# Performance work log

Measured on AMD Instinct MI355X. Metric: run time of the kernel, lower is better.

The kernel has to match this reference:

```python
import jax, jax.numpy as jnp
import numpy as np

EPS = 1e-8  # cosine-similarity epsilon (torch default)


def setup_inputs() -> dict:
    key = jax.random.key(0)
    k1, k2, k3 = jax.random.split(key, 3)
    B, T, D = 256, 512, 512
    video_embedding = jax.random.normal(k1, (B, T, D), dtype=jnp.float32)
    sentence_embedding = jax.random.normal(k2, (B, D), dtype=jnp.float32)
    # valid lengths in [16, T] so no row is fully masked (softmax stays finite)
    video_lengths = jax.random.randint(k3, (B,), 16, T + 1, dtype=jnp.int32)
    return {
        "video_embedding": video_embedding,
        "sentence_embedding": sentence_embedding,
        "video_lengths": video_lengths,
    }


def reference(video_embedding, sentence_embedding, video_lengths):
    B, T, D = video_embedding.shape
    # cosine similarity between every video frame and every sentence -> [B, B, T]
    vn = video_embedding / jnp.maximum(
        jnp.linalg.norm(video_embedding, axis=-1, keepdims=True), EPS)
    sn = sentence_embedding / jnp.maximum(
        jnp.linalg.norm(sentence_embedding, axis=-1, keepdims=True), EPS)
    sim = jnp.einsum("btd,jd->bjt", vn, sn)  # [B_video, B_sent, T]
    # length mask: frames t >= video_lengths[i] get -inf (vectorized version of
    # the original nested python loop)
    valid = jnp.arange(T)[None, None, :] < video_lengths[:, None, None]  # [B,1,T]
    masked = jnp.where(valid, sim, -jnp.inf)
    similarity = jax.nn.softmax(masked, axis=2)  # [B, B, T]
    # argmax over frames, take the diagonal (matched video/sentence pair)
    max_arg = jnp.argmax(similarity, axis=2)       # [B, B]
    diag = jnp.diagonal(max_arg)                   # [B]
    video_max = jnp.take_along_axis(
        video_embedding, diag[:, None, None], axis=1)[:, 0, :]  # [B, D]
    return similarity, video_max
```

## Files before the change

### kernel.cpp

```cpp
#include <hip/hip_runtime.h>
#include <hip/hip_bf16.h>
#include <cstdint>

constexpr int NB = 256;
constexpr int NT = 512;
constexpr int ND = 512;

typedef __attribute__((ext_vector_type(8))) short bf16x8;
typedef __attribute__((ext_vector_type(4))) float f32x4;
typedef __attribute__((ext_vector_type(4))) unsigned int u32x4;

__device__ __forceinline__ float wred_sum(float v){
#pragma unroll
  for (int m = 32; m > 0; m >>= 1) v += __shfl_xor(v, m, 64);
  return v;
}
__device__ __forceinline__ unsigned int f2bf(float f){
  unsigned int u = __builtin_bit_cast(unsigned int, f);
  u = u + 0x7fffu + ((u >> 16) & 1u);
  return (u >> 16);
}
__device__ __forceinline__ void gload_lds16(const void* g, void* l){
  __builtin_amdgcn_global_load_lds(
      (const __attribute__((address_space(1))) unsigned int*)g,
      (__attribute__((address_space(3))) unsigned int*)l, 16, 0, 0);
}

__global__ __launch_bounds__(256) void k_sent(const float* __restrict__ s,
                                              unsigned short* __restrict__ sb,
                                              float* __restrict__ sinv){
  int row  = blockIdx.x * 4 + (threadIdx.x >> 6);
  int lane = threadIdx.x & 63;
  const float* sr = s + (size_t)row * ND;
  float x[8]; float ss = 0.f;
#pragma unroll
  for (int e = 0; e < 8; e++){ x[e] = sr[lane + e*64]; ss += x[e]*x[e]; }
  ss = wred_sum(ss);
  float inv = 1.0f / fmaxf(sqrtf(ss), 1e-8f);
#pragma unroll
  for (int e = 0; e < 8; e++)
    sb[(size_t)row*ND + lane + e*64] = (unsigned short)f2bf(x[e]*inv);
  if (lane == 0) sinv[row] = inv;
}

__global__ __launch_bounds__(256) void k_vnorm(const float* __restrict__ video,
                                               const float* __restrict__ sent,
                                               const float* __restrict__ sinv,
                                               unsigned short* __restrict__ vb16,
                                               float* __restrict__ diag){
  const int tid  = threadIdx.x;
  const int row  = blockIdx.x * 4 + (tid >> 6);
  const int lane = tid & 63;
  const int b    = row >> 9;
  __shared__ float sRowS[ND];
  sRowS[tid]       = sent[(size_t)b*ND + tid];
  sRowS[tid + 256] = sent[(size_t)b*ND + 256 + tid];
  __syncthreads();

  const float* vr = video + (size_t)row * ND;
  f32x4 x0 = *reinterpret_cast<const f32x4*>(vr + lane*8);
  f32x4 x1 = *reinterpret_cast<const f32x4*>(vr + lane*8 + 4);
  float ss = 0.f, dp = 0.f;
#pragma unroll
  for (int i = 0; i < 4; i++){
    ss += x0[i]*x0[i] + x1[i]*x1[i];
    dp += x0[i]*sRowS[lane*8 + i] + x1[i]*sRowS[lane*8 + 4 + i];
  }
#pragma unroll
  for (int m = 32; m > 0; m >>= 1){
    ss += __shfl_xor(ss, m, 64);
    dp += __shfl_xor(dp, m, 64);
  }
  float inv = 1.0f / fmaxf(sqrtf(ss), 1e-8f);
  if (lane == 0) diag[row] = dp * inv * sinv[b];
  u32x4 d;
  d[0] = f2bf(x0[0]*inv) | (f2bf(x0[1]*inv) << 16);
  d[1] = f2bf(x0[2]*inv) | (f2bf(x0[3]*inv) << 16);
  d[2] = f2bf(x1[0]*inv) | (f2bf(x1[1]*inv) << 16);
  d[3] = f2bf(x1[2]*inv) | (f2bf(x1[3]*inv) << 16);
  *reinterpret_cast<u32x4*>(vb16 + (size_t)row*ND + lane*8) = d;
}

__global__ __launch_bounds__(512, 4) void k_gemm_sm(
    const unsigned short* __restrict__ sb,
    const unsigned short* __restrict__ vb16,
    const int* __restrict__ lens,
    float* __restrict__ out0){
  const int tid  = threadIdx.x;
  const int lane = tid & 63;
  const int w    = tid >> 6;
  const int wj   = w >> 2;
  const int wt   = w & 3;

  const int D  = blockIdx.x;
  const int x8 = D & 7;
  const int r0 = D >> 3;
  const int s  = r0 & 3;
  const int b  = (r0 >> 2) * 8 + x8;
  const int jt = s * 64;

  __shared__ __align__(16) unsigned short As[2][64*32];
  __shared__ __align__(16) unsigned short Bs[2][NT*32];
  __shared__ float redM[64*4];
  __shared__ float redS[64*4];

  const unsigned short* vbase = vb16 + (size_t)b * NT * ND;
  const int srow = lane >> 2;
  const int sgr  = ((lane&3) ^ ((lane>>3)&3)) * 8;

  char* AsB = (char*)As;
  char* BsB = (char*)Bs;

  auto STAGE = [&](int buf, int k0){
#pragma unroll
    for (int i = 0; i < 4; i++){
      int grow = w*64 + i*16 + srow;
      gload_lds16(vbase + (size_t)grow*ND + k0 + sgr,
                  BsB + buf*32768 + w*4096 + i*1024 + lane*16);
    }
    if (w < 4){
      int grow = jt + w*16 + srow;
      gload_lds16(sb + (size_t)grow*ND + k0 + sgr,
                  AsB + buf*4096 + w*1024 + lane*16);
    }
  };

  f32x4 acc[2][8] = {};

  STAGE(0, 0);
  asm volatile("s_waitcnt vmcnt(0)" ::: "memory");
  __syncthreads();

  const int rl = lane & 15;
  const int gr = lane >> 4;
  const int goff = ((gr ^ ((rl>>1)&3)) << 4);

  for (int k = 0; k < 16; ++k){
    const int cur = k & 1;
    if (k < 15) STAGE(1-cur, (k+1)*32);
    __builtin_amdgcn_sched_barrier(0);

    bf16x8 af0 = *reinterpret_cast<const bf16x8*>(AsB + cur*4096 + (wj*32 +      rl)*64 + goff);
    bf16x8 af1 = *reinterpret_cast<const bf16x8*>(AsB + cur*4096 + (wj*32 + 16 + rl)*64 + goff);
#pragma unroll
    for (int fj = 0; fj < 8; fj++){
      bf16x8 bg = *reinterpret_cast<const bf16x8*>(BsB + cur*32768 + (wt*128 + fj*16 + rl)*64 + goff);
      acc[0][fj] = __builtin_amdgcn_mfma_f32_16x16x32_bf16(af0, bg, acc[0][fj], 0, 0, 0);
      acc[1][fj] = __builtin_amdgcn_mfma_f32_16x16x32_bf16(af1, bg, acc[1][fj], 0, 0, 0);
    }
    asm volatile("s_waitcnt vmcnt(0)" ::: "memory");
    __syncthreads();
  }

  const int len = lens[b];
  const int q  = gr;
  const int tl = rl;
  const float NEGINF = -__builtin_inff();

  float mx[2][4];
#pragma unroll
  for (int fi = 0; fi < 2; fi++)
#pragma unroll
    for (int rr = 0; rr < 4; rr++) mx[fi][rr] = NEGINF;

#pragma unroll
  for (int fi = 0; fi < 2; fi++)
#pragma unroll
    for (int fj = 0; fj < 8; fj++){
      int t = wt*128 + fj*16 + tl;
      bool ok = t < len;
#pragma unroll
      for (int rr = 0; rr < 4; rr++){
        float v = ok ? acc[fi][fj][rr] : NEGINF;
        acc[fi][fj][rr] = v;
        mx[fi][rr] = fmaxf(mx[fi][rr], v);
      }
    }
#pragma unroll
  for (int fi = 0; fi < 2; fi++)
#pragma unroll
    for (int rr = 0; rr < 4; rr++)
#pragma unroll
      for (int msk = 1; msk <= 8; msk <<= 1)
        mx[fi][rr] = fmaxf(mx[fi][rr], __shfl_xor(mx[fi][rr], msk, 64));
  if (tl == 0){
#pragma unroll
    for (int fi = 0; fi < 2; fi++)
#pragma unroll
      for (int rr = 0; rr < 4; rr++)
        redM[(wj*32 + fi*16 + q*4 + rr)*4 + wt] = mx[fi][rr];
  }
  __syncthreads();

  float gmx[2][4], sum[2][4];
#pragma unroll
  for (int fi = 0; fi < 2; fi++)
#pragma unroll
    for (int rr = 0; rr < 4; rr++){
      int jl = wj*32 + fi*16 + q*4 + rr;
      gmx[fi][rr] = fmaxf(fmaxf(redM[jl*4+0], redM[jl*4+1]),
                          fmaxf(redM[jl*4+2], redM[jl*4+3]));
      sum[fi][rr] = 0.f;
    }
#pragma unroll
  for (int fi = 0; fi < 2; fi++)
#pragma unroll
    for (int fj = 0; fj < 8; fj++)
#pragma unroll
      for (int rr = 0; rr < 4; rr++){
        float e = __expf(acc[fi][fj][rr] - gmx[fi][rr]);
        acc[fi][fj][rr] = e;
        sum[fi][rr] += e;
      }
#pragma unroll
  for (int fi = 0; fi < 2; fi++)
#pragma unroll
    for (int rr = 0; rr < 4; rr++)
#pragma unroll
      for (int msk = 1; msk <= 8; msk <<= 1)
        sum[fi][rr] += __shfl_xor(sum[fi][rr], msk, 64);
  if (tl == 0){
#pragma unroll
    for (int fi = 0; fi < 2; fi++)
#pragma unroll
      for (int rr = 0; rr < 4; rr++)
        redS[(wj*32 + fi*16 + q*4 + rr)*4 + wt] = sum[fi][rr];
  }
  __syncthreads();

#pragma unroll
  for (int fi = 0; fi < 2; fi++)
#pragma unroll
    for (int rr = 0; rr < 4; rr++){
      int jl = wj*32 + fi*16 + q*4 + rr;
      float tot = (redS[jl*4+0] + redS[jl*4+1]) + (redS[jl*4+2] + redS[jl*4+3]);
      float iv = 1.0f / tot;
      int j = jt + jl;
      float* orow = out0 + ((size_t)b*NB + j)*NT + wt*128 + tl;
#pragma unroll
      for (int fj = 0; fj < 8; fj++)
        orow[fj*16] = acc[fi][fj][rr]*iv;
    }
}

__global__ __launch_bounds__(256) void k_argmax(const float* __restrict__ video,
                                                const int* __restrict__ lens,
                                                const float* __restrict__ diag,
                                                float* __restrict__ o1){
  int b = blockIdx.x;
  int tid = threadIdx.x;
  int len = lens[b];
  __shared__ float sv[256];
  __shared__ int   si[256];
  const float* dg = diag + (size_t)b * NT;
  float v1 = (tid       < len) ? dg[tid]       : -__builtin_inff();
  float v2 = (tid + 256 < len) ? dg[tid + 256] : -__builtin_inff();
  float bv; int bi;
  if (v2 > v1){ bv = v2; bi = tid + 256; } else { bv = v1; bi = tid; }
  sv[tid] = bv; si[tid] = bi;
  __syncthreads();
  for (int sN = 128; sN > 0; sN >>= 1){
    if (tid < sN){
      float ov = sv[tid+sN]; int oi = si[tid+sN];
      if (ov > sv[tid] || (ov == sv[tid] && oi < si[tid])){ sv[tid] = ov; si[tid] = oi; }
    }
    __syncthreads();
  }
  int best = si[0];
  const float* src = video + ((size_t)b * NT + best) * ND;
  o1[(size_t)b * ND + tid]       = src[tid];
  o1[(size_t)b * ND + tid + 256] = src[tid + 256];
}

extern "C" void kernel_launch(void* const* d_in, const int* in_sizes, int n_in,
                              void* d_out, int out_size, void* d_ws, size_t ws_size,
                              hipStream_t stream){
  const float* video = (const float*)d_in[0];
  const float* sent  = (const float*)d_in[1];
  const int*   lens  = (const int*)d_in[2];
  float* out0 = (float*)d_out;
  float* out1 = out0 + (size_t)NB*NB*NT;

  char* ws = (char*)d_ws;
  unsigned short* sb   = (unsigned short*)ws;
  float* sinv  = (float*)(ws + 262144);
  float* diagw = (float*)(ws + 263168);
  unsigned short* vb16 = (unsigned short*)(ws + 1048576);

  k_sent   <<<NB/4,    256, 0, stream>>>(sent, sb, sinv);
  k_vnorm  <<<NB*NT/4, 256, 0, stream>>>(video, sent, sinv, vb16, diagw);
  k_gemm_sm<<<NB*4,    512, 0, stream>>>(sb, vb16, lens, out0);
  k_argmax <<<NB,      256, 0, stream>>>(video, lens, diagw, out1);
}
```

Baseline: 169.0 us.

## Stage GEMM output through LDS for coalesced stores and relax K-loop waits

The softmax output tile is now written to a padded shared-memory buffer that reuses the operand staging pool, then stored to global memory as contiguous float4 rows instead of strided scalar stores. The K loop now waits only for the current buffer's loads using partial vmcnt counts and raw s_barrier, so the next stage's loads stay in flight during the MFMAs. The sentence inverse norm is dropped from the diagonal score, since a positive per-row scale does not change the argmax. This adds LDS traffic and extra barriers in the epilogue, and the larger shared pool may reduce occupancy.

```diff
diff --git a/kernel.cpp b/kernel.cpp
--- a/kernel.cpp
+++ b/kernel.cpp
@@ -27,8 +27,7 @@
 }
 
 __global__ __launch_bounds__(256) void k_sent(const float* __restrict__ s,
-                                              unsigned short* __restrict__ sb,
-                                              float* __restrict__ sinv){
+                                              unsigned short* __restrict__ sb){
   int row  = blockIdx.x * 4 + (threadIdx.x >> 6);
   int lane = threadIdx.x & 63;
   const float* sr = s + (size_t)row * ND;
@@ -40,12 +39,10 @@
 #pragma unroll
   for (int e = 0; e < 8; e++)
     sb[(size_t)row*ND + lane + e*64] = (unsigned short)f2bf(x[e]*inv);
-  if (lane == 0) sinv[row] = inv;
 }
 
 __global__ __launch_bounds__(256) void k_vnorm(const float* __restrict__ video,
                                                const float* __restrict__ sent,
-                                               const float* __restrict__ sinv,
                                                unsigned short* __restrict__ vb16,
                                                float* __restrict__ diag){
   const int tid  = threadIdx.x;
@@ -72,7 +69,7 @@
     dp += __shfl_xor(dp, m, 64);
   }
   float inv = 1.0f / fmaxf(sqrtf(ss), 1e-8f);
-  if (lane == 0) diag[row] = dp * inv * sinv[b];
+  if (lane == 0) diag[row] = dp * inv;
   u32x4 d;
   d[0] = f2bf(x0[0]*inv) | (f2bf(x0[1]*inv) << 16);
   d[1] = f2bf(x0[2]*inv) | (f2bf(x0[3]*inv) << 16);
@@ -99,17 +96,16 @@
   const int b  = (r0 >> 2) * 8 + x8;
   const int jt = s * 64;
 
-  __shared__ __align__(16) unsigned short As[2][64*32];
-  __shared__ __align__(16) unsigned short Bs[2][NT*32];
+  __shared__ __align__(16) char pool[73728];
   __shared__ float redM[64*4];
   __shared__ float redS[64*4];
+
+  char* AsB = pool;
+  char* BsB = pool + 8192;
 
   const unsigned short* vbase = vb16 + (size_t)b * NT * ND;
   const int srow = lane >> 2;
   const int sgr  = ((lane&3) ^ ((lane>>3)&3)) * 8;
-
-  char* AsB = (char*)As;
-  char* BsB = (char*)Bs;
 
   auto STAGE = [&](int buf, int k0){
 #pragma unroll
@@ -127,17 +123,23 @@
 
   f32x4 acc[2][8] = {};
 
-  STAGE(0, 0);
-  asm volatile("s_waitcnt vmcnt(0)" ::: "memory");
-  __syncthreads();
-
   const int rl = lane & 15;
   const int gr = lane >> 4;
   const int goff = ((gr ^ ((rl>>1)&3)) << 4);
 
+  STAGE(0, 0);
+
   for (int k = 0; k < 16; ++k){
     const int cur = k & 1;
-    if (k < 15) STAGE(1-cur, (k+1)*32);
+    if (k < 15){
+      STAGE(1-cur, (k+1)*32);
+      if (w < 4) asm volatile("s_waitcnt vmcnt(5)" ::: "memory");
+      else       asm volatile("s_waitcnt vmcnt(4)" ::: "memory");
+    } else {
+      asm volatile("s_waitcnt vmcnt(0)" ::: "memory");
+    }
+    __builtin_amdgcn_s_barrier();
+    asm volatile("" ::: "memory");
     __builtin_amdgcn_sched_barrier(0);
 
     bf16x8 af0 = *reinterpret_cast<const bf16x8*>(AsB + cur*4096 + (wj*32 +      rl)*64 + goff);
@@ -148,8 +150,9 @@
       acc[0][fj] = __builtin_amdgcn_mfma_f32_16x16x32_bf16(af0, bg, acc[0][fj], 0, 0, 0);
       acc[1][fj] = __builtin_amdgcn_mfma_f32_16x16x32_bf16(af1, bg, acc[1][fj], 0, 0, 0);
     }
-    asm volatile("s_waitcnt vmcnt(0)" ::: "memory");
-    __syncthreads();
+    __builtin_amdgcn_sched_barrier(0);
+    asm volatile("" ::: "memory");
+    __builtin_amdgcn_s_barrier();
   }
 
   const int len = lens[b];
@@ -228,19 +231,39 @@
   }
   __syncthreads();
 
+  float ivv[2][4];
 #pragma unroll
   for (int fi = 0; fi < 2; fi++)
 #pragma unroll
     for (int rr = 0; rr < 4; rr++){
       int jl = wj*32 + fi*16 + q*4 + rr;
-      float tot = (redS[jl*4+0] + redS[jl*4+1]) + (redS[jl*4+2] + redS[jl*4+3]);
-      float iv = 1.0f / tot;
-      int j = jt + jl;
-      float* orow = out0 + ((size_t)b*NB + j)*NT + wt*128 + tl;
-#pragma unroll
-      for (int fj = 0; fj < 8; fj++)
-        orow[fj*16] = acc[fi][fj][rr]*iv;
-    }
+      ivv[fi][rr] = 1.0f / ((redS[jl*4+0] + redS[jl*4+1]) + (redS[jl*4+2] + redS[jl*4+3]));
+    }
+
+  float* pf = (float*)pool;
+  const int r2 = tid >> 7;
+  const int c4 = (tid & 127) * 4;
+#pragma unroll
+  for (int fi = 0; fi < 2; fi++){
+    __syncthreads();
+#pragma unroll
+    for (int fj = 0; fj < 8; fj++){
+      int t = wt*128 + fj*16 + tl;
+#pragma unroll
+      for (int rr = 0; rr < 4; rr++){
+        int r = wj*16 + q*4 + rr;
+        pf[r*516 + t] = acc[fi][fj][rr] * ivv[fi][rr];
+      }
+    }
+    __syncthreads();
+#pragma unroll
+    for (int p = 0; p < 8; p++){
+      int row = p*4 + r2;
+      int gj  = jt + ((row >> 4) * 32) + fi*16 + (row & 15);
+      f32x4 vv = *reinterpret_cast<const f32x4*>(pf + row*516 + c4);
+      *reinterpret_cast<f32x4*>(out0 + ((size_t)b*NB + gj)*NT + c4) = vv;
+    }
+  }
 }
 
 __global__ __launch_bounds__(256) void k_argmax(const float* __restrict__ video,
@@ -283,12 +306,11 @@
 
   char* ws = (char*)d_ws;
   unsigned short* sb   = (unsigned short*)ws;
-  float* sinv  = (float*)(ws + 262144);
-  float* diagw = (float*)(ws + 263168);
+  float* diagw = (float*)(ws + 262144);
   unsigned short* vb16 = (unsigned short*)(ws + 1048576);
 
-  k_sent   <<<NB/4,    256, 0, stream>>>(sent, sb, sinv);
-  k_vnorm  <<<NB*NT/4, 256, 0, stream>>>(video, sent, sinv, vb16, diagw);
+  k_sent   <<<NB/4,    256, 0, stream>>>(sent, sb);
+  k_vnorm  <<<NB*NT/4, 256, 0, stream>>>(video, sent, vb16, diagw);
   k_gemm_sm<<<NB*4,    512, 0, stream>>>(sb, vb16, lens, out0);
   k_argmax <<<NB,      256, 0, stream>>>(video, lens, diagw, out1);
 }
```

Result: no change. 169.8 us (+0.4%).
